# Optimization experiments

Measured on AMD Instinct MI355X. Metric: run time of the kernel, lower is better.

## Reference

```python
import jax, jax.numpy as jnp
import numpy as np

NUM_GRAPHS = 128
NODES_PER_GRAPH = 512
LATENT_DIM = 256


def setup_inputs() -> dict:
    key = jax.random.key(0)
    n_total = NUM_GRAPHS * NODES_PER_GRAPH
    z = jax.random.normal(key, (n_total, LATENT_DIM), dtype=jnp.float32)
    # sorted graph assignment: nodes of graph i are contiguous
    batch = (jnp.arange(n_total, dtype=jnp.int32) // NODES_PER_GRAPH).astype(jnp.int32)
    return {"z": z, "batch": batch, "num_graphs": NUM_GRAPHS, "max_nodes": NODES_PER_GRAPH}


def reference(z, batch, num_graphs, max_nodes):
    # Eval-mode forward (dropout is identity when not training).
    n_total, d = z.shape
    ones = jnp.ones((n_total,), dtype=jnp.int32)
    counts = jax.ops.segment_sum(ones, batch, num_segments=num_graphs)  # [G]
    starts = jnp.concatenate([jnp.zeros((1,), jnp.int32), jnp.cumsum(counts)[:-1].astype(jnp.int32)])
    pos = jnp.arange(n_total, dtype=jnp.int32) - starts[batch]  # intra-graph node index
    # Scatter nodes into zero-padded [G, max_nodes, D] tensor
    z_pad = jnp.zeros((num_graphs, max_nodes, d), dtype=z.dtype).at[batch, pos].set(z)
    valid = jnp.zeros((num_graphs, max_nodes), dtype=bool).at[batch, pos].set(True)
    # Per-graph inner-product decoder + sigmoid, padded positions forced to 0
    adj = jax.nn.sigmoid(jnp.einsum('gnd,gmd->gnm', z_pad, z_pad))  # [G, N, N]
    mask = valid[:, :, None] & valid[:, None, :]
    return jnp.where(mask, adj, jnp.zeros((), dtype=adj.dtype))
```

## Files before the change

kernel.cpp:

```cpp
#include <hip/hip_runtime.h>

typedef __fp16 fp16x2 __attribute__((ext_vector_type(2)));
typedef _Float16 half8 __attribute__((ext_vector_type(8)));
typedef float floatx4 __attribute__((ext_vector_type(4)));

namespace {

constexpr int NODES = 512;
constexpr int DIM   = 256;
constexpr int BM    = 128;
constexpr int BKF   = 64;

union Cvt8 { fp16x2 h2[4]; half8 h8; };

__device__ inline half8 pack8(const floatx4 f0, const floatx4 f1) {
  Cvt8 c;
  c.h2[0] = __builtin_amdgcn_cvt_pkrtz(f0.x, f0.y);
  c.h2[1] = __builtin_amdgcn_cvt_pkrtz(f0.z, f0.w);
  c.h2[2] = __builtin_amdgcn_cvt_pkrtz(f1.x, f1.y);
  c.h2[3] = __builtin_amdgcn_cvt_pkrtz(f1.z, f1.w);
  return c.h8;
}

__device__ inline void async_ld16(const void* g, void* lds) {
  __builtin_amdgcn_global_load_lds(
      (const __attribute__((address_space(1))) unsigned int*)g,
      (__attribute__((address_space(3))) unsigned int*)lds,
      16, 0, 0);
}

__device__ inline float sigmoidf(float x) {
  return __builtin_amdgcn_rcpf(1.0f + __expf(-x));
}

__global__ __launch_bounds__(256, 2)
void fused_kernel(const float* __restrict__ z, float* __restrict__ out) {
  __shared__ __align__(16) float As[BM * BKF];
  __shared__ __align__(16) float Bs[BM * BKF];

  const int bid = blockIdx.x;
  const int x    = bid & 7;
  const int j    = bid >> 3;
  const int ggrp = j / 10;
  const int t    = j - ggrp * 10;
  const int g    = x + 8 * ggrp;

  int tn, tm;
  if (t < 4)      { tn = 0; tm = t; }
  else if (t < 7) { tn = 1; tm = t - 3; }
  else if (t < 9) { tn = 2; tm = t - 5; }
  else            { tn = 3; tm = 3; }
  const bool diag = (tn == tm);

  const int tid  = threadIdx.x;
  const int lane = tid & 63;
  const int wave = tid >> 6;
  const int wRow = wave >> 1;
  const int wCol = wave & 1;
  const int lrow = lane & 15;
  const int quad = lane >> 4;

  const float* zA = z + ((size_t)g * NODES + tn * BM) * DIM;
  const float* zB = z + ((size_t)g * NODES + tm * BM) * DIM;

  const int sRowL = lane >> 4;
  const int sC    = lane & 15;

  const float* Bsrc = diag ? As : Bs;

  floatx4 acc[4][4];
#pragma unroll
  for (int i = 0; i < 4; ++i)
#pragma unroll
    for (int jj = 0; jj < 4; ++jj)
      acc[i][jj] = (floatx4){0.f, 0.f, 0.f, 0.f};

  for (int kk = 0; kk < DIM; kk += BKF) {
#pragma unroll
    for (int it = 0; it < 8; ++it) {
      const int q   = wave * 8 + it;
      const int row = q * 4 + sRowL;
      const int cs  = sC ^ (row & 15);
      const size_t srcOff = (size_t)row * DIM + kk + cs * 4;
      async_ld16(zA + srcOff, &As[q * 256]);
      if (!diag) async_ld16(zB + srcOff, &Bs[q * 256]);
    }
    __syncthreads();

#pragma unroll
    for (int ks = 0; ks < 2; ++ks) {
      const int cg0 = ks * 8 + quad * 2;
      half8 af[4], bf[4];
#pragma unroll
      for (int i = 0; i < 4; ++i) {
        const int row = wRow * 64 + i * 16 + lrow;
        const floatx4 a0 = *reinterpret_cast<const floatx4*>(
            &As[row * BKF + ((cg0)     ^ lrow) * 4]);
        const floatx4 a1 = *reinterpret_cast<const floatx4*>(
            &As[row * BKF + ((cg0 + 1) ^ lrow) * 4]);
        af[i] = pack8(a0, a1);
      }
#pragma unroll
      for (int jj = 0; jj < 4; ++jj) {
        const int row = wCol * 64 + jj * 16 + lrow;
        const floatx4 b0 = *reinterpret_cast<const floatx4*>(
            &Bsrc[row * BKF + ((cg0)     ^ lrow) * 4]);
        const floatx4 b1 = *reinterpret_cast<const floatx4*>(
            &Bsrc[row * BKF + ((cg0 + 1) ^ lrow) * 4]);
        bf[jj] = pack8(b0, b1);
      }
#pragma unroll
      for (int i = 0; i < 4; ++i)
#pragma unroll
        for (int jj = 0; jj < 4; ++jj)
          acc[i][jj] = __builtin_amdgcn_mfma_f32_16x16x32_f16(af[i], bf[jj], acc[i][jj], 0, 0, 0);
    }
    __syncthreads();
  }

  float* outg = out + (size_t)g * NODES * NODES;
  const int nBase = tn * BM + wRow * 64;
  const int mBase = tm * BM + wCol * 64;
#pragma unroll
  for (int jj = 0; jj < 4; ++jj) {
    const int m = mBase + jj * 16 + lrow;
    float* rowp = outg + (size_t)m * NODES;
#pragma unroll
    for (int i = 0; i < 4; ++i) {
      const int n0 = nBase + i * 16 + quad * 4;
      floatx4 v;
#pragma unroll
      for (int r = 0; r < 4; ++r)
        v[r] = sigmoidf(acc[i][jj][r]);
      *reinterpret_cast<floatx4*>(rowp + n0) = v;
      if (!diag) {
#pragma unroll
        for (int r = 0; r < 4; ++r)
          outg[(size_t)(n0 + r) * NODES + m] = v[r];
      }
    }
  }
}

}

extern "C" void kernel_launch(void* const* d_in, const int* in_sizes, int n_in,
                              void* d_out, int out_size, void* d_ws, size_t ws_size,
                              hipStream_t stream) {
  const float* z = (const float*)d_in[0];
  float* out = (float*)d_out;
  (void)d_ws; (void)ws_size;
  hipLaunchKernelGGL(fused_kernel, dim3(128 * 10), dim3(256), 0, stream, z, out);
}
```

Before: 193.0 us.

## Double-buffer LDS panels to overlap async global loads with MFMA compute

Halves the K-tile to 32 and uses two ping-pong LDS buffers per operand, so the async global-to-LDS load of the next K panel is issued before computing on the current one. The intent is to hide global load latency behind MFMA work. LDS usage stays the same, so occupancy should be unchanged. The cost is more barriers per K step, and correctness depends on the synchronization between the async loads and the next reads.

```diff
diff --git a/kernel.cpp b/kernel.cpp
--- a/kernel.cpp
+++ b/kernel.cpp
@@ -9,7 +9,8 @@
 constexpr int NODES = 512;
 constexpr int DIM   = 256;
 constexpr int BM    = 128;
-constexpr int BKF   = 64;
+constexpr int BKF   = 32;
+constexpr int PANEL = BM * BKF;
 
 union Cvt8 { fp16x2 h2[4]; half8 h8; };
 
@@ -35,10 +36,10 @@
 
 __global__ __launch_bounds__(256, 2)
 void fused_kernel(const float* __restrict__ z, float* __restrict__ out) {
-  __shared__ __align__(16) float As[BM * BKF];
-  __shared__ __align__(16) float Bs[BM * BKF];
+  __shared__ __align__(16) float As[2 * PANEL];
+  __shared__ __align__(16) float Bs[2 * PANEL];
 
-  const int bid = blockIdx.x;
+  const int bid  = blockIdx.x;
   const int x    = bid & 7;
   const int j    = bid >> 3;
   const int ggrp = j / 10;
@@ -63,10 +64,14 @@
   const float* zA = z + ((size_t)g * NODES + tn * BM) * DIM;
   const float* zB = z + ((size_t)g * NODES + tm * BM) * DIM;
 
-  const int sRowL = lane >> 4;
-  const int sC    = lane & 15;
+  const int    sRow = lane >> 3;
+  const int    sCs  = (lane & 7) ^ sRow;
+  const size_t sOff = (size_t)sRow * DIM + sCs * 4;
 
-  const float* Bsrc = diag ? As : Bs;
+  const int c0 = (quad * 2)     ^ (lrow & 7);
+  const int c1 = (quad * 2 + 1) ^ (lrow & 7);
+  const int rA = (wRow * 64 + lrow) * BKF;
+  const int rB = (wCol * 64 + lrow) * BKF;
 
   floatx4 acc[4][4];
 #pragma unroll
@@ -75,46 +80,53 @@
     for (int jj = 0; jj < 4; ++jj)
       acc[i][jj] = (floatx4){0.f, 0.f, 0.f, 0.f};
 
-  for (int kk = 0; kk < DIM; kk += BKF) {
+  auto stage = [&](int kk, float* dA, float* dB) {
 #pragma unroll
-    for (int it = 0; it < 8; ++it) {
-      const int q   = wave * 8 + it;
-      const int row = q * 4 + sRowL;
-      const int cs  = sC ^ (row & 15);
-      const size_t srcOff = (size_t)row * DIM + kk + cs * 4;
-      async_ld16(zA + srcOff, &As[q * 256]);
-      if (!diag) async_ld16(zB + srcOff, &Bs[q * 256]);
+    for (int it = 0; it < 4; ++it) {
+      const int q = wave * 4 + it;
+      async_ld16(zA + (size_t)q * 8 * DIM + kk + sOff, dA + q * 256);
+      if (!diag)
+        async_ld16(zB + (size_t)q * 8 * DIM + kk + sOff, dB + q * 256);
     }
-    __syncthreads();
+  };
+
+  auto compute = [&](const float* pA, const float* pB) {
+    const float* pBs = diag ? pA : pB;
+    half8 af[4], bf[4];
+#pragma unroll
+    for (int i = 0; i < 4; ++i) {
+      const int base = rA + i * 16 * BKF;
+      const floatx4 a0 = *reinterpret_cast<const floatx4*>(&pA[base + c0 * 4]);
+      const floatx4 a1 = *reinterpret_cast<const floatx4*>(&pA[base + c1 * 4]);
+      af[i] = pack8(a0, a1);
+    }
+#pragma unroll
+    for (int jj = 0; jj < 4; ++jj) {
+      const int base = rB + jj * 16 * BKF;
+      const floatx4 b0 = *reinterpret_cast<const floatx4*>(&pBs[base + c0 * 4]);
+      const floatx4 b1 = *reinterpret_cast<const floatx4*>(&pBs[base + c1 * 4]);
+      bf[jj] = pack8(b0, b1);
+    }
+#pragma unroll
+    for (int i = 0; i < 4; ++i)
+#pragma unroll
+      for (int jj = 0; jj < 4; ++jj)
+        acc[i][jj] = __builtin_amdgcn_mfma_f32_16x16x32_f16(af[i], bf[jj], acc[i][jj], 0, 0, 0);
+  };
+
+  float* A0 = As;  float* A1 = As + PANEL;
+  float* B0 = Bs;  float* B1 = Bs + PANEL;
+
+  stage(0, A0, B0);
+  __syncthreads();
 
 #pragma unroll
-    for (int ks = 0; ks < 2; ++ks) {
-      const int cg0 = ks * 8 + quad * 2;
-      half8 af[4], bf[4];
-#pragma unroll
-      for (int i = 0; i < 4; ++i) {
-        const int row = wRow * 64 + i * 16 + lrow;
-        const floatx4 a0 = *reinterpret_cast<const floatx4*>(
-            &As[row * BKF + ((cg0)     ^ lrow) * 4]);
-        const floatx4 a1 = *reinterpret_cast<const floatx4*>(
-            &As[row * BKF + ((cg0 + 1) ^ lrow) * 4]);
-        af[i] = pack8(a0, a1);
-      }
-#pragma unroll
-      for (int jj = 0; jj < 4; ++jj) {
-        const int row = wCol * 64 + jj * 16 + lrow;
-        const floatx4 b0 = *reinterpret_cast<const floatx4*>(
-            &Bsrc[row * BKF + ((cg0)     ^ lrow) * 4]);
-        const floatx4 b1 = *reinterpret_cast<const floatx4*>(
-            &Bsrc[row * BKF + ((cg0 + 1) ^ lrow) * 4]);
-        bf[jj] = pack8(b0, b1);
-      }
-#pragma unroll
-      for (int i = 0; i < 4; ++i)
-#pragma unroll
-        for (int jj = 0; jj < 4; ++jj)
-          acc[i][jj] = __builtin_amdgcn_mfma_f32_16x16x32_f16(af[i], bf[jj], acc[i][jj], 0, 0, 0);
-    }
+  for (int tt = 0; tt < 4; ++tt) {
+    stage((2 * tt + 1) * BKF, A1, B1);
+    compute(A0, B0);
+    __syncthreads();
+    if (tt < 3) stage((2 * tt + 2) * BKF, A0, B0);
+    compute(A1, B1);
     __syncthreads();
   }
 
```

Measured after the change: 198.1 us. 1.03x slower.

## Load operands directly from global memory into registers, dropping LDS staging

Applied to the files above, without the earlier changes.

Replaces the async global-to-LDS staging and the block-wide barriers with per-lane direct vector loads from global memory into MFMA fragments, fully unrolled over K. It also raises the launch-bounds occupancy hint to three blocks per CU. The goal is to remove barrier and LDS overhead and let more waves overlap. In exchange, waves that share rows now issue redundant global loads that depend on cache hits, and register pressure may rise.

```diff
diff --git a/kernel.cpp b/kernel.cpp
--- a/kernel.cpp
+++ b/kernel.cpp
@@ -9,7 +9,6 @@
 constexpr int NODES = 512;
 constexpr int DIM   = 256;
 constexpr int BM    = 128;
-constexpr int BKF   = 64;
 
 union Cvt8 { fp16x2 h2[4]; half8 h8; };
 
@@ -22,23 +21,13 @@
   return c.h8;
 }
 
-__device__ inline void async_ld16(const void* g, void* lds) {
-  __builtin_amdgcn_global_load_lds(
-      (const __attribute__((address_space(1))) unsigned int*)g,
-      (__attribute__((address_space(3))) unsigned int*)lds,
-      16, 0, 0);
-}
-
 __device__ inline float sigmoidf(float x) {
   return __builtin_amdgcn_rcpf(1.0f + __expf(-x));
 }
 
-__global__ __launch_bounds__(256, 2)
+__global__ __launch_bounds__(256, 3)
 void fused_kernel(const float* __restrict__ z, float* __restrict__ out) {
-  __shared__ __align__(16) float As[BM * BKF];
-  __shared__ __align__(16) float Bs[BM * BKF];
-
-  const int bid = blockIdx.x;
+  const int bid  = blockIdx.x;
   const int x    = bid & 7;
   const int j    = bid >> 3;
   const int ggrp = j / 10;
@@ -60,13 +49,8 @@
   const int lrow = lane & 15;
   const int quad = lane >> 4;
 
-  const float* zA = z + ((size_t)g * NODES + tn * BM) * DIM;
-  const float* zB = z + ((size_t)g * NODES + tm * BM) * DIM;
-
-  const int sRowL = lane >> 4;
-  const int sC    = lane & 15;
-
-  const float* Bsrc = diag ? As : Bs;
+  const float* pA = z + ((size_t)g * NODES + tn * BM + wRow * 64 + lrow) * DIM + quad * 8;
+  const float* pB = z + ((size_t)g * NODES + tm * BM + wCol * 64 + lrow) * DIM + quad * 8;
 
   floatx4 acc[4][4];
 #pragma unroll
@@ -75,47 +59,29 @@
     for (int jj = 0; jj < 4; ++jj)
       acc[i][jj] = (floatx4){0.f, 0.f, 0.f, 0.f};
 
-  for (int kk = 0; kk < DIM; kk += BKF) {
 #pragma unroll
-    for (int it = 0; it < 8; ++it) {
-      const int q   = wave * 8 + it;
-      const int row = q * 4 + sRowL;
-      const int cs  = sC ^ (row & 15);
-      const size_t srcOff = (size_t)row * DIM + kk + cs * 4;
-      async_ld16(zA + srcOff, &As[q * 256]);
-      if (!diag) async_ld16(zB + srcOff, &Bs[q * 256]);
+  for (int kk = 0; kk < 8; ++kk) {
+    const int ko = kk * 32;
+    half8 af[4], bf[4];
+#pragma unroll
+    for (int i = 0; i < 4; ++i) {
+      const float* p = pA + (size_t)i * 16 * DIM + ko;
+      const floatx4 a0 = *reinterpret_cast<const floatx4*>(p);
+      const floatx4 a1 = *reinterpret_cast<const floatx4*>(p + 4);
+      af[i] = pack8(a0, a1);
     }
-    __syncthreads();
-
 #pragma unroll
-    for (int ks = 0; ks < 2; ++ks) {
-      const int cg0 = ks * 8 + quad * 2;
-      half8 af[4], bf[4];
+    for (int jj = 0; jj < 4; ++jj) {
+      const float* p = pB + (size_t)jj * 16 * DIM + ko;
+      const floatx4 b0 = *reinterpret_cast<const floatx4*>(p);
+      const floatx4 b1 = *reinterpret_cast<const floatx4*>(p + 4);
+      bf[jj] = pack8(b0, b1);
+    }
 #pragma unroll
-      for (int i = 0; i < 4; ++i) {
-        const int row = wRow * 64 + i * 16 + lrow;
-        const floatx4 a0 = *reinterpret_cast<const floatx4*>(
-            &As[row * BKF + ((cg0)     ^ lrow) * 4]);
-        const floatx4 a1 = *reinterpret_cast<const floatx4*>(
-            &As[row * BKF + ((cg0 + 1) ^ lrow) * 4]);
-        af[i] = pack8(a0, a1);
-      }
+    for (int i = 0; i < 4; ++i)
 #pragma unroll
-      for (int jj = 0; jj < 4; ++jj) {
-        const int row = wCol * 64 + jj * 16 + lrow;
-        const floatx4 b0 = *reinterpret_cast<const floatx4*>(
-            &Bsrc[row * BKF + ((cg0)     ^ lrow) * 4]);
-        const floatx4 b1 = *reinterpret_cast<const floatx4*>(
-            &Bsrc[row * BKF + ((cg0 + 1) ^ lrow) * 4]);
-        bf[jj] = pack8(b0, b1);
-      }
-#pragma unroll
-      for (int i = 0; i < 4; ++i)
-#pragma unroll
-        for (int jj = 0; jj < 4; ++jj)
-          acc[i][jj] = __builtin_amdgcn_mfma_f32_16x16x32_f16(af[i], bf[jj], acc[i][jj], 0, 0, 0);
-    }
-    __syncthreads();
+      for (int jj = 0; jj < 4; ++jj)
+        acc[i][jj] = __builtin_amdgcn_mfma_f32_16x16x32_f16(af[i], bf[jj], acc[i][jj], 0, 0, 0);
   }
 
   float* outg = out + (size_t)g * NODES * NODES;
```

Result: slower. 257.8 us (+33.6%).
